# Kernel optimization log

Hardware: AMD Instinct MI355X
Metric: run time of the kernel (lower is better)

## Reference

```python
import jax, jax.numpy as jnp
import numpy as np

B, S, D = 2, 2048, 2048
H = 32
HD = D // H  # 64


def setup_inputs() -> dict:
    key = jax.random.key(0)
    ks = jax.random.split(key, 7)
    s = 1.0 / np.sqrt(D)
    return {
        "hidden_states": jax.random.normal(ks[0], (B, S, D), dtype=jnp.float32),
        "Wq": jax.random.normal(ks[1], (D, D), dtype=jnp.float32) * s,
        "Wk": jax.random.normal(ks[2], (D, D), dtype=jnp.float32) * s,
        "Wv": jax.random.normal(ks[3], (D, D), dtype=jnp.float32) * s,
        "Wf": jax.random.normal(ks[4], (H, D), dtype=jnp.float32) * s,
        "bf": jax.random.normal(ks[5], (H,), dtype=jnp.float32) * 0.1,
        "Wo": jax.random.normal(ks[6], (D, D), dtype=jnp.float32) * s,
    }


def _forgetting_attn(x, Wq, Wk, Wv, Wf, bf, Wo):
    b, s, _ = x.shape
    # projections (torch Linear: y = x @ W.T)
    q = (x @ Wq.T).reshape(b, s, H, HD)
    k = (x @ Wk.T).reshape(b, s, H, HD)
    v = (x @ Wv.T).reshape(b, s, H, HD)
    # per-head log-sigmoid forget gates, fp32, cumulative sum over time
    f = jax.nn.log_sigmoid((x @ Wf.T + bf).astype(jnp.float32))  # [b, s, H]
    c = jnp.cumsum(f, axis=1)  # [b, s, H]
    scale = 1.0 / np.sqrt(HD)
    # scores with forget bias: c_i - c_j
    scores = jnp.einsum("bihd,bjhd->bhij", q, k) * scale
    scores = scores + (c[:, :, None, :] - c[:, None, :, :]).transpose(0, 3, 1, 2)
    causal = jnp.tril(jnp.ones((s, s), dtype=bool))
    scores = jnp.where(causal[None, None], scores, -jnp.inf)
    p = jax.nn.softmax(scores, axis=-1)
    o = jnp.einsum("bhij,bjhd->bihd", p, v).reshape(b, s, D)
    return o @ Wo.T


def reference(hidden_states, Wq, Wk, Wv, Wf, bf, Wo):
    return _forgetting_attn(hidden_states, Wq, Wk, Wv, Wf, bf, Wo)
```

## Files before the change

kernel.cpp:

```cpp
#include <hip/hip_runtime.h>
#include <math.h>

#define B 2
#define S 2048
#define D 2048
#define H 32
#define HD 64
#define M (B*S)

typedef short s16x8 __attribute__((ext_vector_type(8)));
typedef float f32x4 __attribute__((ext_vector_type(4)));

__device__ __forceinline__ unsigned short f2bf(float f) {
    unsigned u = __float_as_uint(f);
    return (unsigned short)((u + 0x7fffu + ((u >> 16) & 1u)) >> 16);
}
__device__ __forceinline__ float bf2f(unsigned short h) {
    return __uint_as_float(((unsigned)h) << 16);
}

__global__ __launch_bounds__(256) void split_kernel(
    const float* __restrict__ in, unsigned short* __restrict__ hi,
    unsigned short* __restrict__ lo, int n)
{
    const int idx = (blockIdx.x * 256 + threadIdx.x) * 8;
    if (idx >= n) return;
    float f[8];
    *(float4*)&f[0] = *(const float4*)(in + idx);
    *(float4*)&f[4] = *(const float4*)(in + idx + 4);
    unsigned short h[8], l[8];
    #pragma unroll
    for (int e = 0; e < 8; ++e) {
        h[e] = f2bf(f[e]);
        l[e] = f2bf(f[e] - bf2f(h[e]));
    }
    *(s16x8*)&hi[idx] = *(s16x8*)&h[0];
    *(s16x8*)&lo[idx] = *(s16x8*)&l[0];
}

#define GBM 128
#define GBN 128
#define GBK 32
#define GLD (GBK + 8)

__global__ __launch_bounds__(256) void gemm_pre(
    const unsigned short* __restrict__ Agh, const unsigned short* __restrict__ Agl,
    const unsigned short* __restrict__ Bgh, const unsigned short* __restrict__ Bgl,
    float* __restrict__ Cf, unsigned short* __restrict__ Ch,
    unsigned short* __restrict__ Cl, int Ndim, int Kdim)
{
    __shared__ unsigned short Ah[GBM * GLD], Al[GBM * GLD];
    __shared__ unsigned short Bh[GBN * GLD], Bl[GBN * GLD];
    const int tid = threadIdx.x;
    const int nwg = gridDim.x, cpx = nwg >> 3;
    const int wg = (blockIdx.x & 7) * cpx + (blockIdx.x >> 3);
    const int ntn = Ndim / GBN;
    const int m0 = (wg / ntn) * GBM, n0 = (wg % ntn) * GBN;

    const int row = tid >> 1;
    const int seg = (tid & 1) << 4;
    const size_t abase = (size_t)(m0 + row) * Kdim + seg;
    const size_t bbase = (size_t)(n0 + row) * Kdim + seg;
    const int sbase = row * GLD + seg;

    const int wv = tid >> 6, lane = tid & 63;
    const int wr = (wv >> 1) << 6, wc = (wv & 1) << 6;
    const int fr = lane & 15, ko = (lane >> 4) << 3;

    f32x4 acc[4][4] = {};
    for (int k0 = 0; k0 < Kdim; k0 += GBK) {
        *(s16x8*)&Ah[sbase]     = *(const s16x8*)&Agh[abase + k0];
        *(s16x8*)&Ah[sbase + 8] = *(const s16x8*)&Agh[abase + k0 + 8];
        *(s16x8*)&Al[sbase]     = *(const s16x8*)&Agl[abase + k0];
        *(s16x8*)&Al[sbase + 8] = *(const s16x8*)&Agl[abase + k0 + 8];
        *(s16x8*)&Bh[sbase]     = *(const s16x8*)&Bgh[bbase + k0];
        *(s16x8*)&Bh[sbase + 8] = *(const s16x8*)&Bgh[bbase + k0 + 8];
        *(s16x8*)&Bl[sbase]     = *(const s16x8*)&Bgl[bbase + k0];
        *(s16x8*)&Bl[sbase + 8] = *(const s16x8*)&Bgl[bbase + k0 + 8];
        __syncthreads();
        s16x8 fah[4], fal[4], fbh[4], fbl[4];
        #pragma unroll
        for (int m = 0; m < 4; ++m) {
            const int r = (wr + m * 16 + fr) * GLD + ko;
            fah[m] = *(s16x8*)&Ah[r];
            fal[m] = *(s16x8*)&Al[r];
        }
        #pragma unroll
        for (int n = 0; n < 4; ++n) {
            const int r = (wc + n * 16 + fr) * GLD + ko;
            fbh[n] = *(s16x8*)&Bh[r];
            fbl[n] = *(s16x8*)&Bl[r];
        }
        #pragma unroll
        for (int m = 0; m < 4; ++m)
            #pragma unroll
            for (int n = 0; n < 4; ++n) {
                acc[m][n] = __builtin_amdgcn_mfma_f32_16x16x32_bf16(fah[m], fbh[n], acc[m][n], 0, 0, 0);
                acc[m][n] = __builtin_amdgcn_mfma_f32_16x16x32_bf16(fah[m], fbl[n], acc[m][n], 0, 0, 0);
                acc[m][n] = __builtin_amdgcn_mfma_f32_16x16x32_bf16(fal[m], fbh[n], acc[m][n], 0, 0, 0);
            }
        __syncthreads();
    }
    const int crow0 = m0 + wr + ((lane >> 4) << 2);
    const int ccol0 = n0 + wc + fr;
    #pragma unroll
    for (int m = 0; m < 4; ++m)
        #pragma unroll
        for (int n = 0; n < 4; ++n)
            #pragma unroll
            for (int r = 0; r < 4; ++r) {
                const float c = acc[m][n][r];
                const size_t idx = (size_t)(crow0 + m * 16 + r) * Ndim + ccol0 + n * 16;
                if (Cf) Cf[idx] = c;
                if (Ch) {
                    const unsigned short hh = f2bf(c);
                    Ch[idx] = hh;
                    if (Cl) Cl[idx] = f2bf(c - bf2f(hh));
                }
            }
}

__global__ __launch_bounds__(256) void fgate_kernel(
    const float* __restrict__ x, const float* __restrict__ Wf,
    const float* __restrict__ bfv, float* __restrict__ F)
{
    __shared__ float xs[D];
    const int bs = blockIdx.x;
    const float* xr = x + (size_t)bs * D;
    for (int i = threadIdx.x * 4; i < D; i += 256 * 4)
        *(float4*)&xs[i] = *(const float4*)&xr[i];
    __syncthreads();
    const int wave = threadIdx.x >> 6, lane = threadIdx.x & 63;
    for (int h = wave * 8; h < wave * 8 + 8; ++h) {
        const float* wr = Wf + (size_t)h * D;
        float sum = 0.f;
        for (int i = lane * 4; i < D; i += 64 * 4) {
            float4 w4 = *(const float4*)&wr[i];
            sum += xs[i]*w4.x + xs[i+1]*w4.y + xs[i+2]*w4.z + xs[i+3]*w4.w;
        }
        #pragma unroll
        for (int off = 32; off > 0; off >>= 1) sum += __shfl_down(sum, off);
        if (lane == 0) {
            float z = sum + bfv[h];
            F[(size_t)bs * H + h] = fminf(z, 0.f) - log1pf(expf(-fabsf(z)));
        }
    }
}

__global__ __launch_bounds__(256) void cumsum_kernel(
    const float* __restrict__ F, float* __restrict__ Ct)
{
    const int b = blockIdx.x >> 5;
    const int h = blockIdx.x & 31;
    const float* base = F + (size_t)b * S * H + h;
    float* outb = Ct + (size_t)(b * H + h) * S;
    __shared__ float part[256];
    const int t = threadIdx.x;
    float v[8];
    float run = 0.f;
    #pragma unroll
    for (int i = 0; i < 8; ++i) {
        v[i] = base[(size_t)(t * 8 + i) * H];
        run += v[i];
        v[i] = run;
    }
    part[t] = run;
    __syncthreads();
    for (int off = 1; off < 256; off <<= 1) {
        float add = (t >= off) ? part[t - off] : 0.f;
        __syncthreads();
        part[t] += add;
        __syncthreads();
    }
    const float offs = (t > 0) ? part[t - 1] : 0.f;
    #pragma unroll
    for (int i = 0; i < 8; ++i)
        outb[t * 8 + i] = v[i] + offs;
}

#define QBLK 256
#define NW 8
#define KV 64
#define PLD 72
#define SCALE 0.125f

__global__ __launch_bounds__(512) void attn_mfma3(
    const unsigned short* __restrict__ Qh, const unsigned short* __restrict__ Ql,
    const unsigned short* __restrict__ Kh, const unsigned short* __restrict__ Vh,
    const float* __restrict__ Ct,
    unsigned short* __restrict__ Oh, unsigned short* __restrict__ Ol)
{
    __shared__ unsigned short Ks[KV * PLD];
    __shared__ unsigned short Vt[HD * PLD];
    __shared__ unsigned short Pb[NW * 16 * PLD];
    __shared__ float cj[KV];

    const int qt = (int)gridDim.x - 1 - blockIdx.x;
    const int b = blockIdx.z >> 5, h = blockIdx.z & 31;
    const int q0 = qt * QBLK;
    const int tid = threadIdx.x, wv = tid >> 6, lane = tid & 63;
    const int g = lane >> 4, fr = lane & 15;

    s16x8 qfh[2][2], qfl[2][2];
    {
        const size_t qb = (size_t)(b * S + q0 + wv * 32) * D + h * HD;
        #pragma unroll
        for (int m = 0; m < 2; ++m)
            #pragma unroll
            for (int kd = 0; kd < 2; ++kd) {
                const size_t off = qb + (size_t)(m * 16 + fr) * D + kd * 32 + g * 8;
                qfh[m][kd] = *(const s16x8*)&Qh[off];
                qfl[m][kd] = *(const s16x8*)&Ql[off];
            }
    }

    f32x4 Oa[2][4] = {};
    float mr[2][4], lr[2][4];
    #pragma unroll
    for (int m = 0; m < 2; ++m)
        #pragma unroll
        for (int r = 0; r < 4; ++r) { mr[m][r] = -INFINITY; lr[m][r] = 0.f; }

    const int imax = q0 + wv * 32 + 31;
    const int nj = (q0 + QBLK) / KV;
    unsigned short* Pw = &Pb[wv * 16 * PLD];

    for (int jt = 0; jt < nj; ++jt) {
        const int j0 = jt * KV;
        {
            const int row = tid >> 3;
            const int seg = (tid & 7) << 3;
            const size_t goff = (size_t)(b * S + j0 + row) * D + h * HD + seg;
            *(s16x8*)&Ks[row * PLD + seg] = *(const s16x8*)&Kh[goff];
            s16x8 v0 = *(const s16x8*)&Vh[goff];
            #pragma unroll
            for (int e = 0; e < 8; ++e)
                Vt[(seg + e) * PLD + row] = (unsigned short)v0[e];
            if (tid < KV)
                cj[tid] = Ct[(size_t)(b * H + h) * S + j0 + tid];
        }
        __syncthreads();

        if (j0 <= imax) {
            s16x8 kfr[4][2];
            #pragma unroll
            for (int n = 0; n < 4; ++n)
                #pragma unroll
                for (int kd = 0; kd < 2; ++kd)
                    kfr[n][kd] = *(s16x8*)&Ks[(n * 16 + fr) * PLD + kd * 32 + g * 8];
            f32x4 sa[2][4] = {};
            #pragma unroll
            for (int m = 0; m < 2; ++m)
                #pragma unroll
                for (int n = 0; n < 4; ++n) {
                    #pragma unroll
                    for (int kd = 0; kd < 2; ++kd) {
                        sa[m][n] = __builtin_amdgcn_mfma_f32_16x16x32_bf16(qfh[m][kd], kfr[n][kd], sa[m][n], 0, 0, 0);
                        sa[m][n] = __builtin_amdgcn_mfma_f32_16x16x32_bf16(qfl[m][kd], kfr[n][kd], sa[m][n], 0, 0, 0);
                    }
                }
            float cjr[4];
            #pragma unroll
            for (int n = 0; n < 4; ++n) cjr[n] = cj[fr + 16 * n];
            float sc[2][4][4];
            float tm[2][4];
            #pragma unroll
            for (int m = 0; m < 2; ++m)
                #pragma unroll
                for (int r = 0; r < 4; ++r) tm[m][r] = -INFINITY;
            #pragma unroll
            for (int m = 0; m < 2; ++m)
                #pragma unroll
                for (int n = 0; n < 4; ++n)
                    #pragma unroll
                    for (int r = 0; r < 4; ++r) {
                        const int qrow = q0 + wv * 32 + m * 16 + g * 4 + r;
                        const int jcol = j0 + fr + 16 * n;
                        float s = sa[m][n][r] * SCALE - cjr[n];
                        s = (jcol <= qrow) ? s : -INFINITY;
                        sc[m][n][r] = s;
                        tm[m][r] = fmaxf(tm[m][r], s);
                    }
            #pragma unroll
            for (int m = 0; m < 2; ++m)
                #pragma unroll
                for (int r = 0; r < 4; ++r) {
                    float v = tm[m][r];
                    v = fmaxf(v, __shfl_xor(v, 1));
                    v = fmaxf(v, __shfl_xor(v, 2));
                    v = fmaxf(v, __shfl_xor(v, 4));
                    v = fmaxf(v, __shfl_xor(v, 8));
                    tm[m][r] = v;
                }
            #pragma unroll
            for (int m = 0; m < 2; ++m)
                #pragma unroll
                for (int r = 0; r < 4; ++r) {
                    const float newm = fmaxf(mr[m][r], tm[m][r]);
                    const float corr = __expf(mr[m][r] - newm);
                    mr[m][r] = newm;
                    lr[m][r] *= corr;
                    #pragma unroll
                    for (int n = 0; n < 4; ++n) Oa[m][n][r] *= corr;
                }
            s16x8 vfr[4][2];
            #pragma unroll
            for (int n = 0; n < 4; ++n)
                #pragma unroll
                for (int kj = 0; kj < 2; ++kj)
                    vfr[n][kj] = *(s16x8*)&Vt[(n * 16 + fr) * PLD + kj * 32 + g * 8];
            #pragma unroll
            for (int m = 0; m < 2; ++m) {
                float ps[4];
                #pragma unroll
                for (int r = 0; r < 4; ++r) ps[r] = 0.f;
                #pragma unroll
                for (int n = 0; n < 4; ++n)
                    #pragma unroll
                    for (int r = 0; r < 4; ++r) {
                        const float p = __expf(sc[m][n][r] - mr[m][r]);
                        ps[r] += p;
                        Pw[(g * 4 + r) * PLD + fr + 16 * n] = f2bf(p);
                    }
                #pragma unroll
                for (int r = 0; r < 4; ++r) {
                    float v = ps[r];
                    v += __shfl_xor(v, 1);
                    v += __shfl_xor(v, 2);
                    v += __shfl_xor(v, 4);
                    v += __shfl_xor(v, 8);
                    lr[m][r] += v;
                }
                s16x8 pf[2];
                #pragma unroll
                for (int kj = 0; kj < 2; ++kj)
                    pf[kj] = *(s16x8*)&Pw[fr * PLD + kj * 32 + g * 8];
                #pragma unroll
                for (int n = 0; n < 4; ++n)
                    #pragma unroll
                    for (int kj = 0; kj < 2; ++kj)
                        Oa[m][n] = __builtin_amdgcn_mfma_f32_16x16x32_bf16(pf[kj], vfr[n][kj], Oa[m][n], 0, 0, 0);
            }
        }
        __syncthreads();
    }

    #pragma unroll
    for (int m = 0; m < 2; ++m) {
        float inv[4];
        #pragma unroll
        for (int r = 0; r < 4; ++r) inv[r] = 1.f / lr[m][r];
        const int row_l = lane >> 2;
        const int ch = (lane & 3) << 4;
        const size_t grow = (size_t)(b * S + q0 + wv * 32 + m * 16 + row_l) * D + h * HD + ch;
        #pragma unroll
        for (int n = 0; n < 4; ++n)
            #pragma unroll
            for (int r = 0; r < 4; ++r)
                Pw[(g * 4 + r) * PLD + fr + 16 * n] = f2bf(Oa[m][n][r] * inv[r]);
        *(s16x8*)&Oh[grow]     = *(s16x8*)&Pw[row_l * PLD + ch];
        *(s16x8*)&Oh[grow + 8] = *(s16x8*)&Pw[row_l * PLD + ch + 8];
        #pragma unroll
        for (int n = 0; n < 4; ++n)
            #pragma unroll
            for (int r = 0; r < 4; ++r) {
                const float c = Oa[m][n][r] * inv[r];
                Pw[(g * 4 + r) * PLD + fr + 16 * n] = f2bf(c - bf2f(f2bf(c)));
            }
        *(s16x8*)&Ol[grow]     = *(s16x8*)&Pw[row_l * PLD + ch];
        *(s16x8*)&Ol[grow + 8] = *(s16x8*)&Pw[row_l * PLD + ch + 8];
    }
}

extern "C" void kernel_launch(void* const* d_in, const int* in_sizes, int n_in,
                              void* d_out, int out_size, void* d_ws, size_t ws_size,
                              hipStream_t stream) {
    const float* x  = (const float*)d_in[0];
    const float* Wq = (const float*)d_in[1];
    const float* Wk = (const float*)d_in[2];
    const float* Wv = (const float*)d_in[3];
    const float* Wf = (const float*)d_in[4];
    const float* bf = (const float*)d_in[5];
    const float* Wo = (const float*)d_in[6];
    float* out = (float*)d_out;

    const size_t MD = (size_t)M * D, DD = (size_t)D * D;
    unsigned short* Xh = (unsigned short*)d_ws;
    unsigned short* Xl = Xh + MD;
    unsigned short* Wh = Xl + MD;
    unsigned short* Wl = Wh + DD;
    unsigned short* Qh = Wl + DD;
    unsigned short* Ql = Qh + MD;
    unsigned short* Kh = Ql + MD;
    unsigned short* Vh = Kh + MD;
    float* Fc = (float*)(Vh + MD);
    float* Ct = Fc + (size_t)M * H;
    unsigned short* Oh = Xh;
    unsigned short* Ol = Xl;

    const dim3 blk(256);
    const dim3 ggrid((M / GBM) * (D / GBN));
    const int nMD = (int)MD, nDD = (int)DD;
    const dim3 gsx(nMD / 8 / 256), gsw(nDD / 8 / 256);

    split_kernel<<<gsx, blk, 0, stream>>>(x, Xh, Xl, nMD);
    split_kernel<<<gsw, blk, 0, stream>>>(Wq, Wh, Wl, nDD);
    gemm_pre<<<ggrid, blk, 0, stream>>>(Xh, Xl, Wh, Wl, nullptr, Qh, Ql, D, D);
    split_kernel<<<gsw, blk, 0, stream>>>(Wk, Wh, Wl, nDD);
    gemm_pre<<<ggrid, blk, 0, stream>>>(Xh, Xl, Wh, Wl, nullptr, Kh, nullptr, D, D);
    split_kernel<<<gsw, blk, 0, stream>>>(Wv, Wh, Wl, nDD);
    gemm_pre<<<ggrid, blk, 0, stream>>>(Xh, Xl, Wh, Wl, nullptr, Vh, nullptr, D, D);
    fgate_kernel<<<dim3(M), blk, 0, stream>>>(x, Wf, bf, Fc);
    cumsum_kernel<<<dim3(B * H), blk, 0, stream>>>(Fc, Ct);
    attn_mfma3<<<dim3(S / QBLK, 1, B * H), dim3(512), 0, stream>>>(Qh, Ql, Kh, Vh, Ct, Oh, Ol);
    split_kernel<<<gsw, blk, 0, stream>>>(Wo, Wh, Wl, nDD);
    gemm_pre<<<ggrid, blk, 0, stream>>>(Oh, Ol, Wh, Wl, out, nullptr, nullptr, D, D);
}
```

Baseline: 898.3 us.

## Drop bf16x3 split for QKV projections and split attention KV range in two

The Q/K/V projection GEMMs now run single-pass bf16 instead of the three-term hi/lo compensated product, which removes two thirds of their MFMA work and the low-part loads. Q also loses its low part in attention. The attention kernel splits each query tile's key range into two halves on separate blocks, writing unnormalized partial outputs plus max and sum statistics. A new merge kernel combines them. This adds parallelism for the causal tail but costs extra memory traffic and a kernel launch, and the reduced precision may hurt accuracy.

```diff
diff --git a/kernel.cpp b/kernel.cpp
--- a/kernel.cpp
+++ b/kernel.cpp
@@ -7,6 +7,7 @@
 #define H 32
 #define HD 64
 #define M (B*S)
+#define MH ((size_t)M * H)
 
 typedef short s16x8 __attribute__((ext_vector_type(8)));
 typedef float f32x4 __attribute__((ext_vector_type(4)));
@@ -35,7 +36,7 @@
         l[e] = f2bf(f[e] - bf2f(h[e]));
     }
     *(s16x8*)&hi[idx] = *(s16x8*)&h[0];
-    *(s16x8*)&lo[idx] = *(s16x8*)&l[0];
+    if (lo) *(s16x8*)&lo[idx] = *(s16x8*)&l[0];
 }
 
 #define GBM 128
@@ -51,6 +52,7 @@
 {
     __shared__ unsigned short Ah[GBM * GLD], Al[GBM * GLD];
     __shared__ unsigned short Bh[GBN * GLD], Bl[GBN * GLD];
+    const bool ulo = (Agl != nullptr);
     const int tid = threadIdx.x;
     const int nwg = gridDim.x, cpx = nwg >> 3;
     const int wg = (blockIdx.x & 7) * cpx + (blockIdx.x >> 3);
@@ -71,33 +73,37 @@
     for (int k0 = 0; k0 < Kdim; k0 += GBK) {
         *(s16x8*)&Ah[sbase]     = *(const s16x8*)&Agh[abase + k0];
         *(s16x8*)&Ah[sbase + 8] = *(const s16x8*)&Agh[abase + k0 + 8];
-        *(s16x8*)&Al[sbase]     = *(const s16x8*)&Agl[abase + k0];
-        *(s16x8*)&Al[sbase + 8] = *(const s16x8*)&Agl[abase + k0 + 8];
         *(s16x8*)&Bh[sbase]     = *(const s16x8*)&Bgh[bbase + k0];
         *(s16x8*)&Bh[sbase + 8] = *(const s16x8*)&Bgh[bbase + k0 + 8];
-        *(s16x8*)&Bl[sbase]     = *(const s16x8*)&Bgl[bbase + k0];
-        *(s16x8*)&Bl[sbase + 8] = *(const s16x8*)&Bgl[bbase + k0 + 8];
+        if (ulo) {
+            *(s16x8*)&Al[sbase]     = *(const s16x8*)&Agl[abase + k0];
+            *(s16x8*)&Al[sbase + 8] = *(const s16x8*)&Agl[abase + k0 + 8];
+            *(s16x8*)&Bl[sbase]     = *(const s16x8*)&Bgl[bbase + k0];
+            *(s16x8*)&Bl[sbase + 8] = *(const s16x8*)&Bgl[bbase + k0 + 8];
+        }
         __syncthreads();
         s16x8 fah[4], fal[4], fbh[4], fbl[4];
         #pragma unroll
         for (int m = 0; m < 4; ++m) {
             const int r = (wr + m * 16 + fr) * GLD + ko;
             fah[m] = *(s16x8*)&Ah[r];
-            fal[m] = *(s16x8*)&Al[r];
+            if (ulo) fal[m] = *(s16x8*)&Al[r];
         }
         #pragma unroll
         for (int n = 0; n < 4; ++n) {
             const int r = (wc + n * 16 + fr) * GLD + ko;
             fbh[n] = *(s16x8*)&Bh[r];
-            fbl[n] = *(s16x8*)&Bl[r];
+            if (ulo) fbl[n] = *(s16x8*)&Bl[r];
         }
         #pragma unroll
         for (int m = 0; m < 4; ++m)
             #pragma unroll
             for (int n = 0; n < 4; ++n) {
                 acc[m][n] = __builtin_amdgcn_mfma_f32_16x16x32_bf16(fah[m], fbh[n], acc[m][n], 0, 0, 0);
-                acc[m][n] = __builtin_amdgcn_mfma_f32_16x16x32_bf16(fah[m], fbl[n], acc[m][n], 0, 0, 0);
-                acc[m][n] = __builtin_amdgcn_mfma_f32_16x16x32_bf16(fal[m], fbh[n], acc[m][n], 0, 0, 0);
+                if (ulo) {
+                    acc[m][n] = __builtin_amdgcn_mfma_f32_16x16x32_bf16(fah[m], fbl[n], acc[m][n], 0, 0, 0);
+                    acc[m][n] = __builtin_amdgcn_mfma_f32_16x16x32_bf16(fal[m], fbh[n], acc[m][n], 0, 0, 0);
+                }
             }
         __syncthreads();
     }
@@ -179,39 +185,43 @@
 }
 
 #define QBLK 256
+#define NTILES (S / QBLK)
 #define NW 8
 #define KV 64
 #define PLD 72
 #define SCALE 0.125f
 
-__global__ __launch_bounds__(512) void attn_mfma3(
-    const unsigned short* __restrict__ Qh, const unsigned short* __restrict__ Ql,
+__global__ __launch_bounds__(512) void attn_mfma4(
+    const unsigned short* __restrict__ Qh,
     const unsigned short* __restrict__ Kh, const unsigned short* __restrict__ Vh,
     const float* __restrict__ Ct,
-    unsigned short* __restrict__ Oh, unsigned short* __restrict__ Ol)
+    unsigned short* __restrict__ P0h, unsigned short* __restrict__ P0l,
+    unsigned short* __restrict__ P1h, unsigned short* __restrict__ P1l,
+    float* __restrict__ ML)
 {
     __shared__ unsigned short Ks[KV * PLD];
     __shared__ unsigned short Vt[HD * PLD];
     __shared__ unsigned short Pb[NW * 16 * PLD];
     __shared__ float cj[KV];
 
-    const int qt = (int)gridDim.x - 1 - blockIdx.x;
+    const int qt = NTILES - 1 - (int)blockIdx.x;
+    const int sp = blockIdx.y;
     const int b = blockIdx.z >> 5, h = blockIdx.z & 31;
     const int q0 = qt * QBLK;
     const int tid = threadIdx.x, wv = tid >> 6, lane = tid & 63;
     const int g = lane >> 4, fr = lane & 15;
-
-    s16x8 qfh[2][2], qfl[2][2];
+    unsigned short* Oph = sp ? P1h : P0h;
+    unsigned short* Opl = sp ? P1l : P0l;
+    float* MLp = ML + (size_t)sp * MH * 2;
+
+    s16x8 qfh[2][2];
     {
         const size_t qb = (size_t)(b * S + q0 + wv * 32) * D + h * HD;
         #pragma unroll
         for (int m = 0; m < 2; ++m)
             #pragma unroll
-            for (int kd = 0; kd < 2; ++kd) {
-                const size_t off = qb + (size_t)(m * 16 + fr) * D + kd * 32 + g * 8;
-                qfh[m][kd] = *(const s16x8*)&Qh[off];
-                qfl[m][kd] = *(const s16x8*)&Ql[off];
-            }
+            for (int kd = 0; kd < 2; ++kd)
+                qfh[m][kd] = *(const s16x8*)&Qh[qb + (size_t)(m * 16 + fr) * D + kd * 32 + g * 8];
     }
 
     f32x4 Oa[2][4] = {};
@@ -222,10 +232,11 @@
         for (int r = 0; r < 4; ++r) { mr[m][r] = -INFINITY; lr[m][r] = 0.f; }
 
     const int imax = q0 + wv * 32 + 31;
-    const int nj = (q0 + QBLK) / KV;
+    const int half = (q0 + QBLK) / KV / 2;
+    const int t0 = sp * half, t1 = t0 + half;
     unsigned short* Pw = &Pb[wv * 16 * PLD];
 
-    for (int jt = 0; jt < nj; ++jt) {
+    for (int jt = t0; jt < t1; ++jt) {
         const int j0 = jt * KV;
         {
             const int row = tid >> 3;
@@ -252,13 +263,10 @@
             #pragma unroll
             for (int m = 0; m < 2; ++m)
                 #pragma unroll
-                for (int n = 0; n < 4; ++n) {
+                for (int n = 0; n < 4; ++n)
                     #pragma unroll
-                    for (int kd = 0; kd < 2; ++kd) {
+                    for (int kd = 0; kd < 2; ++kd)
                         sa[m][n] = __builtin_amdgcn_mfma_f32_16x16x32_bf16(qfh[m][kd], kfr[n][kd], sa[m][n], 0, 0, 0);
-                        sa[m][n] = __builtin_amdgcn_mfma_f32_16x16x32_bf16(qfl[m][kd], kfr[n][kd], sa[m][n], 0, 0, 0);
-                    }
-                }
             float cjr[4];
             #pragma unroll
             for (int n = 0; n < 4; ++n) cjr[n] = cj[fr + 16 * n];
@@ -347,9 +355,6 @@
 
     #pragma unroll
     for (int m = 0; m < 2; ++m) {
-        float inv[4];
-        #pragma unroll
-        for (int r = 0; r < 4; ++r) inv[r] = 1.f / lr[m][r];
         const int row_l = lane >> 2;
         const int ch = (lane & 3) << 4;
         const size_t grow = (size_t)(b * S + q0 + wv * 32 + m * 16 + row_l) * D + h * HD + ch;
@@ -357,19 +362,55 @@
         for (int n = 0; n < 4; ++n)
             #pragma unroll
             for (int r = 0; r < 4; ++r)
-                Pw[(g * 4 + r) * PLD + fr + 16 * n] = f2bf(Oa[m][n][r] * inv[r]);
-        *(s16x8*)&Oh[grow]     = *(s16x8*)&Pw[row_l * PLD + ch];
-        *(s16x8*)&Oh[grow + 8] = *(s16x8*)&Pw[row_l * PLD + ch + 8];
+                Pw[(g * 4 + r) * PLD + fr + 16 * n] = f2bf(Oa[m][n][r]);
+        *(s16x8*)&Oph[grow]     = *(s16x8*)&Pw[row_l * PLD + ch];
+        *(s16x8*)&Oph[grow + 8] = *(s16x8*)&Pw[row_l * PLD + ch + 8];
         #pragma unroll
         for (int n = 0; n < 4; ++n)
             #pragma unroll
             for (int r = 0; r < 4; ++r) {
-                const float c = Oa[m][n][r] * inv[r];
+                const float c = Oa[m][n][r];
                 Pw[(g * 4 + r) * PLD + fr + 16 * n] = f2bf(c - bf2f(f2bf(c)));
             }
-        *(s16x8*)&Ol[grow]     = *(s16x8*)&Pw[row_l * PLD + ch];
-        *(s16x8*)&Ol[grow + 8] = *(s16x8*)&Pw[row_l * PLD + ch + 8];
-    }
+        *(s16x8*)&Opl[grow]     = *(s16x8*)&Pw[row_l * PLD + ch];
+        *(s16x8*)&Opl[grow + 8] = *(s16x8*)&Pw[row_l * PLD + ch + 8];
+        if (fr == 0)
+            #pragma unroll
+            for (int r = 0; r < 4; ++r) {
+                const size_t row = (size_t)(b * S + q0 + wv * 32 + m * 16 + g * 4 + r);
+                MLp[(row * H + h) * 2]     = mr[m][r];
+                MLp[(row * H + h) * 2 + 1] = lr[m][r];
+            }
+    }
+}
+
+__global__ __launch_bounds__(256) void merge_kernel(
+    unsigned short* __restrict__ P0h, unsigned short* __restrict__ P0l,
+    const unsigned short* __restrict__ P1h, const unsigned short* __restrict__ P1l,
+    const float* __restrict__ ML)
+{
+    const size_t t8 = ((size_t)blockIdx.x * 256 + threadIdx.x) * 8;
+    const size_t r = t8 / D;
+    const int h = (int)((t8 % D) / HD);
+    const size_t mlb = (r * H + h) * 2;
+    const float m0 = ML[mlb],            l0 = ML[mlb + 1];
+    const float m1 = ML[MH * 2 + mlb],   l1 = ML[MH * 2 + mlb + 1];
+    const float mx = fmaxf(m0, m1);
+    const float w0 = __expf(m0 - mx), w1 = __expf(m1 - mx);
+    const float inv = 1.f / (w0 * l0 + w1 * l1);
+    s16x8 a0 = *(const s16x8*)&P0h[t8], b0 = *(const s16x8*)&P0l[t8];
+    s16x8 a1 = *(const s16x8*)&P1h[t8], b1 = *(const s16x8*)&P1l[t8];
+    unsigned short oh[8], ol[8];
+    #pragma unroll
+    for (int e = 0; e < 8; ++e) {
+        const float v0 = bf2f((unsigned short)a0[e]) + bf2f((unsigned short)b0[e]);
+        const float v1 = bf2f((unsigned short)a1[e]) + bf2f((unsigned short)b1[e]);
+        const float o = (w0 * v0 + w1 * v1) * inv;
+        oh[e] = f2bf(o);
+        ol[e] = f2bf(o - bf2f(oh[e]));
+    }
+    *(s16x8*)&P0h[t8] = *(s16x8*)&oh[0];
+    *(s16x8*)&P0l[t8] = *(s16x8*)&ol[0];
 }
 
 extern "C" void kernel_launch(void* const* d_in, const int* in_sizes, int n_in,
@@ -386,33 +427,35 @@
 
     const size_t MD = (size_t)M * D, DD = (size_t)D * D;
     unsigned short* Xh = (unsigned short*)d_ws;
-    unsigned short* Xl = Xh + MD;
-    unsigned short* Wh = Xl + MD;
+    unsigned short* Wh = Xh + MD;
     unsigned short* Wl = Wh + DD;
     unsigned short* Qh = Wl + DD;
-    unsigned short* Ql = Qh + MD;
-    unsigned short* Kh = Ql + MD;
+    unsigned short* Kh = Qh + MD;
     unsigned short* Vh = Kh + MD;
     float* Fc = (float*)(Vh + MD);
-    float* Ct = Fc + (size_t)M * H;
-    unsigned short* Oh = Xh;
-    unsigned short* Ol = Xl;
+    float* Ct = Fc + MH;
+    unsigned short* P0l = (unsigned short*)(Ct + MH);
+    unsigned short* P1h = P0l + MD;
+    unsigned short* P1l = P1h + MD;
+    float* ML = (float*)(P1l + MD);
+    unsigned short* P0h = Xh;
 
     const dim3 blk(256);
     const dim3 ggrid((M / GBM) * (D / GBN));
     const int nMD = (int)MD, nDD = (int)DD;
     const dim3 gsx(nMD / 8 / 256), gsw(nDD / 8 / 256);
 
-    split_kernel<<<gsx, blk, 0, stream>>>(x, Xh, Xl, nMD);
-    split_kernel<<<gsw, blk, 0, stream>>>(Wq, Wh, Wl, nDD);
-    gemm_pre<<<ggrid, blk, 0, stream>>>(Xh, Xl, Wh, Wl, nullptr, Qh, Ql, D, D);
-    split_kernel<<<gsw, blk, 0, stream>>>(Wk, Wh, Wl, nDD);
-    gemm_pre<<<ggrid, blk, 0, stream>>>(Xh, Xl, Wh, Wl, nullptr, Kh, nullptr, D, D);
-    split_kernel<<<gsw, blk, 0, stream>>>(Wv, Wh, Wl, nDD);
-    gemm_pre<<<ggrid, blk, 0, stream>>>(Xh, Xl, Wh, Wl, nullptr, Vh, nullptr, D, D);
+    split_kernel<<<gsx, blk, 0, stream>>>(x, Xh, nullptr, nMD);
+    split_kernel<<<gsw, blk, 0, stream>>>(Wq, Wh, nullptr, nDD);
+    gemm_pre<<<ggrid, blk, 0, stream>>>(Xh, nullptr, Wh, nullptr, nullptr, Qh, nullptr, D, D);
+    split_kernel<<<gsw, blk, 0, stream>>>(Wk, Wh, nullptr, nDD);
+    gemm_pre<<<ggrid, blk, 0, stream>>>(Xh, nullptr, Wh, nullptr, nullptr, Kh, nullptr, D, D);
+    split_kernel<<<gsw, blk, 0, stream>>>(Wv, Wh, nullptr, nDD);
+    gemm_pre<<<ggrid, blk, 0, stream>>>(Xh, nullptr, Wh, nullptr, nullptr, Vh, nullptr, D, D);
     fgate_kernel<<<dim3(M), blk, 0, stream>>>(x, Wf, bf, Fc);
     cumsum_kernel<<<dim3(B * H), blk, 0, stream>>>(Fc, Ct);
-    attn_mfma3<<<dim3(S / QBLK, 1, B * H), dim3(512), 0, stream>>>(Qh, Ql, Kh, Vh, Ct, Oh, Ol);
+    attn_mfma4<<<dim3(NTILES, 2, B * H), dim3(512), 0, stream>>>(Qh, Kh, Vh, Ct, P0h, P0l, P1h, P1l, ML);
+    merge_kernel<<<dim3((int)(MD / 8 / 256)), blk, 0, stream>>>(P0h, P0l, P1h, P1l, ML);
     split_kernel<<<gsw, blk, 0, stream>>>(Wo, Wh, Wl, nDD);
-    gemm_pre<<<ggrid, blk, 0, stream>>>(Oh, Ol, Wh, Wl, out, nullptr, nullptr, D, D);
-}
+    gemm_pre<<<ggrid, blk, 0, stream>>>(P0h, P0l, Wh, Wl, out, nullptr, nullptr, D, D);
+}
```

Result: faster. 822.0 us (-8.5%).
